# Performance work log

Hardware: AMD Instinct MI355X
Metric: run time of the kernel (lower is better)

## Reference

```python
import jax, jax.numpy as jnp
import numpy as np

N, E, IN_FT, OUT_FT = 8192, 4096, 512, 512
DENSITY = 0.02


def setup_inputs() -> dict:
    key = jax.random.key(0)
    k1, k2, k3, k4 = jax.random.split(key, 4)
    x = jax.random.normal(k1, (N, IN_FT), dtype=jnp.float32)
    hypergraph = (jax.random.uniform(k2, (N, E)) < DENSITY).astype(jnp.float32)
    # kaiming_uniform on [in, out]: fan_in = in_ft (torch fan of a Linear-style 2D param is dim 1 size? torch computes fan_in = size(1) for 2D -> out_ft here)
    bound_w = float(np.sqrt(6.0 / OUT_FT))  # kaiming_uniform a=sqrt(5)? default a=0 -> gain sqrt(2); bound = gain*sqrt(3/fan_in)
    bound_w = float(np.sqrt(2.0) * np.sqrt(3.0 / OUT_FT))
    weight = jax.random.uniform(k3, (IN_FT, OUT_FT), minval=-bound_w, maxval=bound_w, dtype=jnp.float32)
    bound_v = float(np.sqrt(2.0) * np.sqrt(3.0 / 1.0))
    V = jax.random.uniform(k4, (IN_FT, 1), minval=-bound_v, maxval=bound_v, dtype=jnp.float32)
    bias = jnp.zeros((OUT_FT,), dtype=jnp.float32)
    return {"x": x, "hypergraph": hypergraph, "weight": weight, "V": V, "bias": bias}


def reference(x, hypergraph, weight, V, bias):
    # edge embeddings: H^T @ x  -> [E, in_ft]
    edge_emb = hypergraph.T @ x
    hw = jax.nn.sigmoid(edge_emb @ V)          # [E, 1] learned hyperedge weights
    w = hw[:, 0]                                # [E]
    deg_v = (hypergraph @ hw)[:, 0]             # [N]  (sum over last dim of H @ hw)
    deg_e = jnp.sum(hypergraph, axis=0)         # [E]
    # adj = diag(deg_v) @ H @ diag(w) @ diag(deg_e) @ H^T @ diag(deg_v)
    # fused as broadcasted row/col scalings around two GEMMs (same math, no NxN)
    out = x @ weight                            # [N, out_ft]
    t = hypergraph.T @ (deg_v[:, None] * out)   # [E, out_ft]
    t = (w * deg_e)[:, None] * t                # diagonal edge scalings
    out = deg_v[:, None] * (hypergraph @ t)     # [N, out_ft]
    out = out + bias
    return (out, w)
```

## Files before the change

### kernel.cpp

```cpp
#include <hip/hip_runtime.h>


#define N_NODES 8192
#define N_EDGES 4096
#define FT 512

typedef short bf16x8 __attribute__((ext_vector_type(8)));
typedef float f32x4 __attribute__((ext_vector_type(4)));
typedef unsigned short u16;
typedef unsigned int u32;

__device__ __forceinline__ u16 f2b(float f) {
    union { float f; u32 u; } v; v.f = f;
    u32 r = v.u + 0x7FFFu + ((v.u >> 16) & 1u);
    return (u16)(r >> 16);
}
__device__ __forceinline__ float b2f(u16 h) {
    union { u32 u; float f; } v; v.u = ((u32)h) << 16; return v.f;
}


__global__ __launch_bounds__(256) void zero_kernel(float* p, int n) {
    int i = blockIdx.x * 256 + threadIdx.x;
    if (i < n) p[i] = 0.f;
}

__global__ __launch_bounds__(256) void xv_xb_kernel(const float* __restrict__ x,
                                                    const float* __restrict__ V,
                                                    float* __restrict__ xv,
                                                    u16* __restrict__ xb) {
    int row = blockIdx.x * 4 + (threadIdx.x >> 6);
    int lane = threadIdx.x & 63;
    const float* xr = x + (size_t)row * FT + lane * 8;
    const float* vr = V + lane * 8;
    float4 a0 = *(const float4*)xr, a1 = *(const float4*)(xr + 4);
    float4 b0 = *(const float4*)vr, b1 = *(const float4*)(vr + 4);
    float acc = a0.x * b0.x + a0.y * b0.y + a0.z * b0.z + a0.w * b0.w +
                a1.x * b1.x + a1.y * b1.y + a1.z * b1.z + a1.w * b1.w;
    u16 tmp[8] = {f2b(a0.x), f2b(a0.y), f2b(a0.z), f2b(a0.w),
                  f2b(a1.x), f2b(a1.y), f2b(a1.z), f2b(a1.w)};
    *(uint4*)(xb + (size_t)row * FT + lane * 8) = *(uint4*)tmp;
#pragma unroll
    for (int off = 32; off; off >>= 1) acc += __shfl_down(acc, off);
    if (lane == 0) xv[row] = acc;
}

__global__ __launch_bounds__(256) void prep_h_kernel(const float* __restrict__ H,
                                                     const float* __restrict__ xv,
                                                     u16* __restrict__ Hbf,
                                                     u16* __restrict__ HTbf,
                                                     float* __restrict__ zsum,
                                                     float* __restrict__ desum) {
    __shared__ u32 Wt[64][33];
    const int t = threadIdx.x;
    const int e0 = blockIdx.x * 64, n0 = blockIdx.y * 64;
    {
        int n = t >> 2, seg = t & 3;
        const float* src = H + (size_t)(n0 + n) * N_EDGES + e0 + seg * 16;
        u16* hdst = Hbf + (size_t)(n0 + n) * N_EDGES + e0 + seg * 16;
        u32 o[8];
#pragma unroll
        for (int j = 0; j < 4; j++) {
            float4 h = *(const float4*)(src + j * 4);
            o[2 * j]     = (h.x != 0.f ? 0x3F80u : 0u) | (h.y != 0.f ? 0x3F800000u : 0u);
            o[2 * j + 1] = (h.z != 0.f ? 0x3F80u : 0u) | (h.w != 0.f ? 0x3F800000u : 0u);
        }
        *(uint4*)hdst       = *(uint4*)&o[0];
        *(uint4*)(hdst + 8) = *(uint4*)&o[4];
#pragma unroll
        for (int j = 0; j < 8; j++) Wt[n][seg * 8 + j] = o[j];
    }
    __syncthreads();
    {
        int e = t >> 2, g = t & 3;
        int ew = e >> 1;
        u32 sel = (e & 1) ? 0x07060302u : 0x05040100u;
        u32 oo[8];
        float z = 0.f, d = 0.f;
#pragma unroll
        for (int j = 0; j < 8; j++) {
            int np = g * 8 + j;
            oo[j] = __builtin_amdgcn_perm(Wt[2 * np + 1][ew], Wt[2 * np][ew], sel);
            if (oo[j] & 0xFFFFu)  { z += xv[n0 + 2 * np];     d += 1.f; }
            if (oo[j] >> 16)      { z += xv[n0 + 2 * np + 1]; d += 1.f; }
        }
        u32* drow = (u32*)(HTbf + (size_t)(e0 + e) * N_NODES + n0);
        *(uint4*)(drow + g * 8)     = *(uint4*)&oo[0];
        *(uint4*)(drow + g * 8 + 4) = *(uint4*)&oo[4];
        z += __shfl_down(z, 2); z += __shfl_down(z, 1);
        d += __shfl_down(d, 2); d += __shfl_down(d, 1);
        if (g == 0) {
            atomicAdd(zsum + e0 + e, z);
            atomicAdd(desum + e0 + e, d);
        }
    }
}

__global__ __launch_bounds__(256) void sigmoid_kernel(const float* __restrict__ zsum,
                                                      const float* __restrict__ desum,
                                                      float* __restrict__ w_out,
                                                      float* __restrict__ wde) {
    int e = blockIdx.x * 256 + threadIdx.x;
    float z = zsum[e];
    float wv = 1.f / (1.f + expf(-z));
    w_out[e] = wv;
    wde[e] = wv * desum[e];
}

__global__ __launch_bounds__(256) void degv_kernel(const u16* __restrict__ Hbf,
                                                   const float* __restrict__ w,
                                                   float* __restrict__ degv) {
    int row = blockIdx.x * 4 + (threadIdx.x >> 6);
    int lane = threadIdx.x & 63;
    const uint4* hr = (const uint4*)(Hbf + (size_t)row * N_EDGES);
    float acc = 0.f;
#pragma unroll
    for (int i = 0; i < 8; i++) {
        int idx = i * 64 + lane;
        uint4 h = hr[idx];
        const float* w8 = w + idx * 8;
        float4 wa = *(const float4*)w8, wb = *(const float4*)(w8 + 4);
        if (h.x & 0xFFFFu) acc += wa.x;  if (h.x >> 16) acc += wa.y;
        if (h.y & 0xFFFFu) acc += wa.z;  if (h.y >> 16) acc += wa.w;
        if (h.z & 0xFFFFu) acc += wb.x;  if (h.z >> 16) acc += wb.y;
        if (h.w & 0xFFFFu) acc += wb.z;  if (h.w >> 16) acc += wb.w;
    }
#pragma unroll
    for (int off = 32; off; off >>= 1) acc += __shfl_down(acc, off);
    if (lane == 0) degv[row] = acc;
}

__global__ void wt_kernel(const float* __restrict__ src, u16* __restrict__ dst) {
    __shared__ float tile[32][33];
    int tx = threadIdx.x, ty = threadIdx.y;
    int c = blockIdx.x * 32 + tx;
    int r0 = blockIdx.y * 32;
#pragma unroll
    for (int i = 0; i < 4; i++)
        tile[ty + i * 8][tx] = src[(size_t)(r0 + ty + i * 8) * FT + c];
    __syncthreads();
#pragma unroll
    for (int i = 0; i < 4; i++)
        dst[(size_t)(blockIdx.x * 32 + ty + i * 8) * FT + r0 + tx] = f2b(tile[tx][ty + i * 8]);
}

__global__ void t2t_kernel(const u16* __restrict__ P, const float* __restrict__ wde,
                           u16* __restrict__ t2T) {
    __shared__ float tile[32][33];
    int tx = threadIdx.x, ty = threadIdx.y;
    int f0 = blockIdx.x * 32, e0 = blockIdx.y * 32;
#pragma unroll
    for (int i = 0; i < 4; i++) {
        int e = e0 + ty + i * 8;
        size_t idx = (size_t)e * 512 + f0 + tx;
        float s = 0.f;
#pragma unroll
        for (int sl = 0; sl < 8; sl++)
            s += b2f(P[idx + (size_t)sl * N_EDGES * 512]);
        tile[ty + i * 8][tx] = wde[e] * s;
    }
    __syncthreads();
#pragma unroll
    for (int i = 0; i < 4; i++)
        t2T[(size_t)(f0 + ty + i * 8) * N_EDGES + e0 + tx] = f2b(tile[tx][ty + i * 8]);
}

__global__ __launch_bounds__(256) void final_kernel(const u16* __restrict__ P,
                                                    const float* __restrict__ degv,
                                                    const float* __restrict__ bias,
                                                    float* __restrict__ out) {
    int i8 = blockIdx.x * 256 + threadIdx.x;
    int base = i8 * 8;
    int n = base >> 9, f = base & 511;
    float s[8] = {0.f, 0.f, 0.f, 0.f, 0.f, 0.f, 0.f, 0.f};
#pragma unroll
    for (int sl = 0; sl < 4; sl++) {
        uint4 v = *(const uint4*)(P + (size_t)sl * N_NODES * 512 + base);
        u32 ws[4] = {v.x, v.y, v.z, v.w};
#pragma unroll
        for (int j = 0; j < 4; j++) {
            s[2 * j]     += b2f((u16)(ws[j] & 0xFFFFu));
            s[2 * j + 1] += b2f((u16)(ws[j] >> 16));
        }
    }
    float dv = degv[n];
    float4 o0, o1;
    o0.x = dv * s[0] + bias[f + 0]; o0.y = dv * s[1] + bias[f + 1];
    o0.z = dv * s[2] + bias[f + 2]; o0.w = dv * s[3] + bias[f + 3];
    o1.x = dv * s[4] + bias[f + 4]; o1.y = dv * s[5] + bias[f + 5];
    o1.z = dv * s[6] + bias[f + 6]; o1.w = dv * s[7] + bias[f + 7];
    *(float4*)(out + base) = o0;
    *(float4*)(out + base + 4) = o1;
}


#define TBK 32

template <int MT, int NT, int EPI>
__global__ __launch_bounds__(256, 3)
void gemm7(const u16* __restrict__ Ap, const u16* __restrict__ Bp,
           void* __restrict__ Cp, const float* __restrict__ degv,
           int KC, int lda, int ldb, int ldc, int Msz) {
    __shared__ __align__(16) u16 Alds[MT * 32 * TBK];
    __shared__ __align__(16) u16 Blds[NT * 32 * TBK];
    const int t = threadIdx.x;
    const int m0 = blockIdx.x * (MT * 32), n0 = blockIdx.y * (NT * 32);
    const int kbase = blockIdx.z * KC;
    const int wave = t >> 6, lane = t & 63, quad = lane >> 4, lo = lane & 15;
    const int wm = (wave >> 1) * (MT * 16), wn = (wave & 1) * (NT * 16);

    f32x4 acc[MT][NT];
#pragma unroll
    for (int a = 0; a < MT; a++)
#pragma unroll
        for (int b = 0; b < NT; b++) acc[a][b] = (f32x4){0.f, 0.f, 0.f, 0.f};

    for (int kk = 0; kk < KC; kk += TBK) {
        const int k0 = kbase + kk;
        __syncthreads();
#pragma unroll
        for (int i = 0; i < MT / 2; i++) {
            int c = t + i * 256;
            int q = ((c & 3) - (c >> 3)) & 3;
            const u16* g = Ap + (size_t)(m0 + (c >> 2)) * lda + k0 + q * 8;
            __builtin_amdgcn_global_load_lds((const u32*)g, (u32*)(Alds + c * 8), 16, 0, 0);
        }
#pragma unroll
        for (int i = 0; i < NT / 2; i++) {
            int c = t + i * 256;
            int q = ((c & 3) - (c >> 3)) & 3;
            const u16* g = Bp + (size_t)(n0 + (c >> 2)) * ldb + k0 + q * 8;
            __builtin_amdgcn_global_load_lds((const u32*)g, (u32*)(Blds + c * 8), 16, 0, 0);
        }
        __syncthreads();

        bf16x8 af[MT], bfr[NT];
#pragma unroll
        for (int mt = 0; mt < MT; mt++) {
            int m = wm + mt * 16 + lo;
            int s = (quad + (m >> 1)) & 3;
            af[mt] = *(const bf16x8*)&Alds[m * TBK + s * 8];
        }
#pragma unroll
        for (int nt = 0; nt < NT; nt++) {
            int n = wn + nt * 16 + lo;
            int s = (quad + (n >> 1)) & 3;
            bfr[nt] = *(const bf16x8*)&Blds[n * TBK + s * 8];
        }
#pragma unroll
        for (int mt = 0; mt < MT; mt++)
#pragma unroll
            for (int nt = 0; nt < NT; nt++)
                acc[mt][nt] = __builtin_amdgcn_mfma_f32_16x16x32_bf16(af[mt], bfr[nt], acc[mt][nt], 0, 0, 0);
    }

    if (EPI == 0) {
        u16* C = (u16*)Cp + (size_t)blockIdx.z * Msz * 512;
#pragma unroll
        for (int mt = 0; mt < MT; mt++) {
            int rb = m0 + wm + mt * 16 + quad * 4;
#pragma unroll
            for (int i = 0; i < 4; i++)
#pragma unroll
                for (int nt = 0; nt < NT; nt++)
                    C[(size_t)(rb + i) * 512 + n0 + wn + nt * 16 + lo] = f2b(acc[mt][nt][i]);
        }
    } else {
        u16* C = (u16*)Cp;
        float dv[NT];
#pragma unroll
        for (int nt = 0; nt < NT; nt++) dv[nt] = degv[n0 + wn + nt * 16 + lo];
#pragma unroll
        for (int mt = 0; mt < MT; mt++) {
            int rb = m0 + wm + mt * 16 + quad * 4;
#pragma unroll
            for (int i = 0; i < 4; i++)
#pragma unroll
                for (int nt = 0; nt < NT; nt++)
                    C[(size_t)(rb + i) * ldc + n0 + wn + nt * 16 + lo] =
                        f2b(acc[mt][nt][i] * dv[nt]);
        }
    }
}


extern "C" void kernel_launch(void* const* d_in, const int* in_sizes, int n_in,
                              void* d_out, int out_size, void* d_ws, size_t ws_size,
                              hipStream_t stream) {
    const float* x    = (const float*)d_in[0];
    const float* H    = (const float*)d_in[1];
    const float* W    = (const float*)d_in[2];
    const float* V    = (const float*)d_in[3];
    const float* bias = (const float*)d_in[4];
    float* out  = (float*)d_out;
    float* wout = out + (size_t)N_NODES * FT;
    (void)in_sizes; (void)n_in; (void)out_size; (void)ws_size;

    char* wsb = (char*)d_ws;
    float* wsf   = (float*)d_ws;
    float* xv    = wsf;
    float* zsum  = wsf + 8192;
    float* desum = wsf + 12288;
    float* wde   = wsf + 16384;
    float* degv  = wsf + 20480;
    u16*   Hbf   = (u16*)(wsb + 114688);
    u16*   HTbf  = (u16*)(wsb + 67223552);
    u16*   WT    = (u16*)(wsb + 134332416);
    u16*   doutT = (u16*)(wsb + 134856704);
    u16*   t2T   = (u16*)(wsb + 143245312);
    u16*   xb    = (u16*)(wsb + 147439616);
    u16*   P     = (u16*)(wsb + 155828224);

    zero_kernel<<<32, 256, 0, stream>>>(zsum, 8192);
    xv_xb_kernel<<<N_NODES / 4, 256, 0, stream>>>(x, V, xv, xb);
    prep_h_kernel<<<dim3(N_EDGES / 64, N_NODES / 64), 256, 0, stream>>>(
        H, xv, Hbf, HTbf, zsum, desum);
    sigmoid_kernel<<<N_EDGES / 256, 256, 0, stream>>>(zsum, desum, wout, wde);
    degv_kernel<<<N_NODES / 4, 256, 0, stream>>>(Hbf, wout, degv);
    wt_kernel<<<dim3(16, 16), dim3(32, 8), 0, stream>>>(W, WT);

    gemm7<2, 4, 1><<<dim3(FT / 64, N_NODES / 128, 1), 256, 0, stream>>>(
        WT, xb, doutT, degv, FT, FT, FT, N_NODES, 0);

    gemm7<4, 4, 0><<<dim3(N_EDGES / 128, FT / 128, 8), 256, 0, stream>>>(
        HTbf, doutT, P, nullptr, N_NODES / 8, N_NODES, N_NODES, 512, N_EDGES);

    t2t_kernel<<<dim3(FT / 32, N_EDGES / 32), dim3(32, 8), 0, stream>>>(P, wde, t2T);

    gemm7<4, 4, 0><<<dim3(N_NODES / 128, FT / 128, 4), 256, 0, stream>>>(
        Hbf, t2T, P, nullptr, N_EDGES / 4, N_EDGES, N_EDGES, 512, N_NODES);

    final_kernel<<<(N_NODES * FT / 8) / 256, 256, 0, stream>>>(P, degv, bias, out);
}
```

Measured before the change: 376.5 us.

## Double GEMM K-tile to 64 with 8-way LDS swizzle; branchless prep reductions

The bf16 MFMA GEMM now stages 64-wide K slices per iteration instead of 32. Each slice is loaded with an 8-chunk rotated swizzle and consumed in two MFMA sub-steps, which halves the number of barrier-separated load/compute rounds. The launch-bounds occupancy hint rises from 3 to 4 blocks, although LDS per block doubles, which may limit residency. The prep_h kernel caches xv in shared memory, and both it and degv use select-based accumulation instead of branches. The workspace offsets for degv and wde are also rearranged.

```diff
diff --git a/kernel.cpp b/kernel.cpp
--- a/kernel.cpp
+++ b/kernel.cpp
@@ -45,15 +45,17 @@
     if (lane == 0) xv[row] = acc;
 }
 
-__global__ __launch_bounds__(256) void prep_h_kernel(const float* __restrict__ H,
-                                                     const float* __restrict__ xv,
-                                                     u16* __restrict__ Hbf,
-                                                     u16* __restrict__ HTbf,
-                                                     float* __restrict__ zsum,
-                                                     float* __restrict__ desum) {
+__global__ __launch_bounds__(256) void prep_h2_kernel(const float* __restrict__ H,
+                                                      const float* __restrict__ xv,
+                                                      u16* __restrict__ Hbf,
+                                                      u16* __restrict__ HTbf,
+                                                      float* __restrict__ zsum,
+                                                      float* __restrict__ desum) {
     __shared__ u32 Wt[64][33];
+    __shared__ float xvs[64];
     const int t = threadIdx.x;
     const int e0 = blockIdx.x * 64, n0 = blockIdx.y * 64;
+    if (t < 64) xvs[t] = xv[n0 + t];
     {
         int n = t >> 2, seg = t & 3;
         const float* src = H + (size_t)(n0 + n) * N_EDGES + e0 + seg * 16;
@@ -81,8 +83,10 @@
         for (int j = 0; j < 8; j++) {
             int np = g * 8 + j;
             oo[j] = __builtin_amdgcn_perm(Wt[2 * np + 1][ew], Wt[2 * np][ew], sel);
-            if (oo[j] & 0xFFFFu)  { z += xv[n0 + 2 * np];     d += 1.f; }
-            if (oo[j] >> 16)      { z += xv[n0 + 2 * np + 1]; d += 1.f; }
+            z += (oo[j] & 0xFFFFu) ? xvs[2 * np] : 0.f;
+            d += (oo[j] & 0xFFFFu) ? 1.f : 0.f;
+            z += (oo[j] >> 16) ? xvs[2 * np + 1] : 0.f;
+            d += (oo[j] >> 16) ? 1.f : 0.f;
         }
         u32* drow = (u32*)(HTbf + (size_t)(e0 + e) * N_NODES + n0);
         *(uint4*)(drow + g * 8)     = *(uint4*)&oo[0];
@@ -120,10 +124,10 @@
         uint4 h = hr[idx];
         const float* w8 = w + idx * 8;
         float4 wa = *(const float4*)w8, wb = *(const float4*)(w8 + 4);
-        if (h.x & 0xFFFFu) acc += wa.x;  if (h.x >> 16) acc += wa.y;
-        if (h.y & 0xFFFFu) acc += wa.z;  if (h.y >> 16) acc += wa.w;
-        if (h.z & 0xFFFFu) acc += wb.x;  if (h.z >> 16) acc += wb.y;
-        if (h.w & 0xFFFFu) acc += wb.z;  if (h.w >> 16) acc += wb.w;
+        acc += (h.x & 0xFFFFu) ? wa.x : 0.f;  acc += (h.x >> 16) ? wa.y : 0.f;
+        acc += (h.y & 0xFFFFu) ? wa.z : 0.f;  acc += (h.y >> 16) ? wa.w : 0.f;
+        acc += (h.z & 0xFFFFu) ? wb.x : 0.f;  acc += (h.z >> 16) ? wb.y : 0.f;
+        acc += (h.w & 0xFFFFu) ? wb.z : 0.f;  acc += (h.w >> 16) ? wb.w : 0.f;
     }
 #pragma unroll
     for (int off = 32; off; off >>= 1) acc += __shfl_down(acc, off);
@@ -194,13 +198,13 @@
 }
 
 
-#define TBK 32
+#define TBK 64
 
 template <int MT, int NT, int EPI>
-__global__ __launch_bounds__(256, 3)
-void gemm7(const u16* __restrict__ Ap, const u16* __restrict__ Bp,
+__global__ __launch_bounds__(256, 4)
+void gemm9(const u16* __restrict__ Ap, const u16* __restrict__ Bp,
            void* __restrict__ Cp, const float* __restrict__ degv,
-           int KC, int lda, int ldb, int ldc, int Msz) {
+           int KC, int lda, int ldb, int ldc, size_t Ssz) {
     __shared__ __align__(16) u16 Alds[MT * 32 * TBK];
     __shared__ __align__(16) u16 Blds[NT * 32 * TBK];
     const int t = threadIdx.x;
@@ -219,43 +223,48 @@
         const int k0 = kbase + kk;
         __syncthreads();
 #pragma unroll
-        for (int i = 0; i < MT / 2; i++) {
+        for (int i = 0; i < MT; i++) {
             int c = t + i * 256;
-            int q = ((c & 3) - (c >> 3)) & 3;
-            const u16* g = Ap + (size_t)(m0 + (c >> 2)) * lda + k0 + q * 8;
+            int r = c >> 3;
+            int j = ((c & 7) - r) & 7;
+            const u16* g = Ap + (size_t)(m0 + r) * lda + k0 + j * 8;
             __builtin_amdgcn_global_load_lds((const u32*)g, (u32*)(Alds + c * 8), 16, 0, 0);
         }
 #pragma unroll
-        for (int i = 0; i < NT / 2; i++) {
+        for (int i = 0; i < NT; i++) {
             int c = t + i * 256;
-            int q = ((c & 3) - (c >> 3)) & 3;
-            const u16* g = Bp + (size_t)(n0 + (c >> 2)) * ldb + k0 + q * 8;
+            int r = c >> 3;
+            int j = ((c & 7) - r) & 7;
+            const u16* g = Bp + (size_t)(n0 + r) * ldb + k0 + j * 8;
             __builtin_amdgcn_global_load_lds((const u32*)g, (u32*)(Blds + c * 8), 16, 0, 0);
         }
         __syncthreads();
 
-        bf16x8 af[MT], bfr[NT];
-#pragma unroll
-        for (int mt = 0; mt < MT; mt++) {
-            int m = wm + mt * 16 + lo;
-            int s = (quad + (m >> 1)) & 3;
-            af[mt] = *(const bf16x8*)&Alds[m * TBK + s * 8];
-        }
-#pragma unroll
-        for (int nt = 0; nt < NT; nt++) {
-            int n = wn + nt * 16 + lo;
-            int s = (quad + (n >> 1)) & 3;
-            bfr[nt] = *(const bf16x8*)&Blds[n * TBK + s * 8];
-        }
-#pragma unroll
-        for (int mt = 0; mt < MT; mt++)
-#pragma unroll
-            for (int nt = 0; nt < NT; nt++)
-                acc[mt][nt] = __builtin_amdgcn_mfma_f32_16x16x32_bf16(af[mt], bfr[nt], acc[mt][nt], 0, 0, 0);
+#pragma unroll
+        for (int s2 = 0; s2 < 2; s2++) {
+            bf16x8 af[MT], bfr[NT];
+#pragma unroll
+            for (int mt = 0; mt < MT; mt++) {
+                int m = wm + mt * 16 + lo;
+                int s = (s2 * 4 + quad + m) & 7;
+                af[mt] = *(const bf16x8*)&Alds[m * TBK + s * 8];
+            }
+#pragma unroll
+            for (int nt = 0; nt < NT; nt++) {
+                int n = wn + nt * 16 + lo;
+                int s = (s2 * 4 + quad + n) & 7;
+                bfr[nt] = *(const bf16x8*)&Blds[n * TBK + s * 8];
+            }
+#pragma unroll
+            for (int mt = 0; mt < MT; mt++)
+#pragma unroll
+                for (int nt = 0; nt < NT; nt++)
+                    acc[mt][nt] = __builtin_amdgcn_mfma_f32_16x16x32_bf16(af[mt], bfr[nt], acc[mt][nt], 0, 0, 0);
+        }
     }
 
     if (EPI == 0) {
-        u16* C = (u16*)Cp + (size_t)blockIdx.z * Msz * 512;
+        u16* C = (u16*)Cp + (size_t)blockIdx.z * Ssz;
 #pragma unroll
         for (int mt = 0; mt < MT; mt++) {
             int rb = m0 + wm + mt * 16 + quad * 4;
@@ -263,7 +272,7 @@
             for (int i = 0; i < 4; i++)
 #pragma unroll
                 for (int nt = 0; nt < NT; nt++)
-                    C[(size_t)(rb + i) * 512 + n0 + wn + nt * 16 + lo] = f2b(acc[mt][nt][i]);
+                    C[(size_t)(rb + i) * ldc + n0 + wn + nt * 16 + lo] = f2b(acc[mt][nt][i]);
         }
     } else {
         u16* C = (u16*)Cp;
@@ -301,8 +310,8 @@
     float* xv    = wsf;
     float* zsum  = wsf + 8192;
     float* desum = wsf + 12288;
-    float* wde   = wsf + 16384;
-    float* degv  = wsf + 20480;
+    float* degv  = wsf + 16384;
+    float* wde   = wsf + 24576;
     u16*   Hbf   = (u16*)(wsb + 114688);
     u16*   HTbf  = (u16*)(wsb + 67223552);
     u16*   WT    = (u16*)(wsb + 134332416);
@@ -313,22 +322,22 @@
 
     zero_kernel<<<32, 256, 0, stream>>>(zsum, 8192);
     xv_xb_kernel<<<N_NODES / 4, 256, 0, stream>>>(x, V, xv, xb);
-    prep_h_kernel<<<dim3(N_EDGES / 64, N_NODES / 64), 256, 0, stream>>>(
+    prep_h2_kernel<<<dim3(N_EDGES / 64, N_NODES / 64), 256, 0, stream>>>(
         H, xv, Hbf, HTbf, zsum, desum);
     sigmoid_kernel<<<N_EDGES / 256, 256, 0, stream>>>(zsum, desum, wout, wde);
     degv_kernel<<<N_NODES / 4, 256, 0, stream>>>(Hbf, wout, degv);
     wt_kernel<<<dim3(16, 16), dim3(32, 8), 0, stream>>>(W, WT);
 
-    gemm7<2, 4, 1><<<dim3(FT / 64, N_NODES / 128, 1), 256, 0, stream>>>(
+    gemm9<2, 4, 1><<<dim3(FT / 64, N_NODES / 128, 1), 256, 0, stream>>>(
         WT, xb, doutT, degv, FT, FT, FT, N_NODES, 0);
 
-    gemm7<4, 4, 0><<<dim3(N_EDGES / 128, FT / 128, 8), 256, 0, stream>>>(
-        HTbf, doutT, P, nullptr, N_NODES / 8, N_NODES, N_NODES, 512, N_EDGES);
+    gemm9<4, 4, 0><<<dim3(N_EDGES / 128, FT / 128, 8), 256, 0, stream>>>(
+        HTbf, doutT, P, nullptr, N_NODES / 8, N_NODES, N_NODES, 512, (size_t)N_EDGES * 512);
 
     t2t_kernel<<<dim3(FT / 32, N_EDGES / 32), dim3(32, 8), 0, stream>>>(P, wde, t2T);
 
-    gemm7<4, 4, 0><<<dim3(N_NODES / 128, FT / 128, 4), 256, 0, stream>>>(
-        Hbf, t2T, P, nullptr, N_EDGES / 4, N_EDGES, N_EDGES, 512, N_NODES);
+    gemm9<4, 4, 0><<<dim3(N_NODES / 128, FT / 128, 4), 256, 0, stream>>>(
+        Hbf, t2T, P, nullptr, N_EDGES / 4, N_EDGES, N_EDGES, 512, (size_t)N_NODES * 512);
 
     final_kernel<<<(N_NODES * FT / 8) / 256, 256, 0, stream>>>(P, degv, bias, out);
 }
```

Result: faster. 359.2 us (-4.6%).
